# Kernel optimization log

Hardware: AMD Instinct MI355X
Metric: run time of the kernel (lower is better)

Reference implementation:

```python
import jax, jax.numpy as jnp
import numpy as np

LOTRI2MAT = np.array([[0, 1, 3], [1, 2, 4], [3, 4, 5]])  # lower-tri 6-vec -> symmetric 3x3
MAT2LOTRI_I = np.array([0, 1, 1, 2, 2, 2])
MAT2LOTRI_J = np.array([0, 0, 1, 0, 1, 2])


def trilinear_warp_border(img, ddf):
    """MONAI Warp(mode='bilinear', padding_mode='border', align_corners=True).
    img: (B,C,H,W,D), ddf: (B,3,H,W,D) displacement in voxel units.
    Samples img at x + ddf(x), clamping coords to the volume (border padding).
    """
    B, C, H, W, D = img.shape
    base = jnp.stack(
        jnp.meshgrid(jnp.arange(H), jnp.arange(W), jnp.arange(D), indexing='ij'),
        axis=0,
    ).astype(img.dtype)  # (3,H,W,D)
    coords = ddf + base[None]  # (B,3,H,W,D)
    x = jnp.clip(coords[:, 0], 0.0, H - 1)
    y = jnp.clip(coords[:, 1], 0.0, W - 1)
    z = jnp.clip(coords[:, 2], 0.0, D - 1)

    x0f, y0f, z0f = jnp.floor(x), jnp.floor(y), jnp.floor(z)
    fx, fy, fz = x - x0f, y - y0f, z - z0f
    x0 = jnp.clip(x0f.astype(jnp.int32), 0, H - 1)
    y0 = jnp.clip(y0f.astype(jnp.int32), 0, W - 1)
    z0 = jnp.clip(z0f.astype(jnp.int32), 0, D - 1)
    x1 = jnp.minimum(x0 + 1, H - 1)
    y1 = jnp.minimum(y0 + 1, W - 1)
    z1 = jnp.minimum(z0 + 1, D - 1)

    def gather(img_b, xi, yi, zi):
        flat = (xi * W + yi) * D + zi  # (H,W,D)
        return img_b.reshape(C, -1)[:, flat.reshape(-1)].reshape(C, H, W, D)

    g = jax.vmap(gather)  # over batch

    out = jnp.zeros_like(img)
    for xi, wx in ((x0, 1.0 - fx), (x1, fx)):
        for yi, wy in ((y0, 1.0 - fy), (y1, fy)):
            for zi, wz in ((z0, 1.0 - fz), (z1, fz)):
                out = out + g(img, xi, yi, zi) * (wx * wy * wz)[:, None]
    return out


def jacobian_of_ddf(ddf):
    """J = I + du/dx via central differences (one-sided at boundaries).
    ddf: (B,3,H,W,D) -> (B,H,W,D,3,3) with J[...,i,j] = d u_i / d x_j + delta_ij."""
    grads = jnp.gradient(ddf, axis=(2, 3, 4))  # list over j of (B,3,H,W,D)
    J = jnp.stack(grads, axis=2)  # (B,3(i),3(j),H,W,D)
    J = J + jnp.eye(3, dtype=ddf.dtype)[None, :, :, None, None, None]
    return jnp.transpose(J, (0, 3, 4, 5, 1, 2))  # (B,H,W,D,3,3)


def setup_inputs() -> dict:
    key = jax.random.key(0)
    k1, k2 = jax.random.split(key)
    dti = jax.random.normal(k1, (2, 6, 64, 64, 64), dtype=jnp.float32)
    ddf = jax.random.normal(k2, (2, 3, 64, 64, 64), dtype=jnp.float32)
    return {"dti": dti, "ddf": ddf}


def reference(dti, ddf):
    b, _, h, w, d = dti.shape
    # 1) trilinear warp of the 6-channel lower-tri DTI
    dti_warped = trilinear_warp_border(dti, ddf)  # (B,6,H,W,D)
    # 2) lower-tri -> full symmetric 3x3, spatial-last
    M = dti_warped[:, LOTRI2MAT]                      # (B,3,3,H,W,D)
    M = jnp.transpose(M, (0, 3, 4, 5, 1, 2))          # (B,H,W,D,3,3)
    # 3) Jacobian of the deformation and its polar-decomposition rotation (finite strain)
    J = jacobian_of_ddf(ddf)                          # (B,H,W,D,3,3)
    U, _, Vh = jnp.linalg.svd(J, full_matrices=False)
    R = jnp.matmul(U, Vh)                             # orthogonal factor of J
    # 4) rotate tensors: R^T M R
    out = jnp.einsum('...ji,...jk,...kl->...il', R, M, R)
    # 5) back to lower-tri channel-first form
    out = jnp.transpose(out, (0, 4, 5, 1, 2, 3))      # (B,3,3,H,W,D)
    return out[:, MAT2LOTRI_I, MAT2LOTRI_J]           # (B,6,H,W,D)
```

## Files before the change

kernel.cpp:

```cpp
#include <hip/hip_runtime.h>

#define NVOX 262144
#define TOTAL (2 * NVOX)

typedef float f2u __attribute__((ext_vector_type(2), aligned(4)));

__global__ __launch_bounds__(256, 8)
void warp_main(const float* __restrict__ dti,
               const float* __restrict__ ddf,
               float* __restrict__ out,
               int* __restrict__ bad, int max_bad)
{
    const int idx = blockIdx.x * 256 + threadIdx.x;
    const int b = idx >> 18;
    const int r = idx & (NVOX - 1);
    const int x = r >> 12;
    const int y = (r >> 6) & 63;
    const int z = r & 63;

    const float* db = ddf + (size_t)b * 3 * NVOX;

    const float ux = db[r];
    const float uy = db[NVOX + r];
    const float uz = db[2 * NVOX + r];

    const float cx = fminf(fmaxf((float)x + ux, 0.0f), 63.0f);
    const float cy = fminf(fmaxf((float)y + uy, 0.0f), 63.0f);
    const float cz = fminf(fmaxf((float)z + uz, 0.0f), 63.0f);
    const float fx0 = floorf(cx), fy0 = floorf(cy), fz0 = floorf(cz);
    const float fx = cx - fx0, fy = cy - fy0, fz = cz - fz0;
    const int x0 = (int)fx0, y0 = (int)fy0, z0 = (int)fz0;
    const int x1 = min(x0 + 1, 63), y1 = min(y0 + 1, 63);

    const float gx = 1.0f - fx, gy = 1.0f - fy, gz = 1.0f - fz;
    const float q00 = gx * gy, q01 = gx * fy, q10 = fx * gy, q11 = fx * fy;

    const bool ztop = (z0 == 63);
    const int zb = ztop ? 62 : z0;
    const int p00 = (x0 * 64 + y0) * 64 + zb, p01 = (x0 * 64 + y1) * 64 + zb;
    const int p10 = (x1 * 64 + y0) * 64 + zb, p11 = (x1 * 64 + y1) * 64 + zb;

    const float* tb = dti + (size_t)b * 6 * NVOX;
    float m[6];
#pragma unroll
    for (int c = 0; c < 6; ++c) {
        const float* tc = tb + c * NVOX;
        const f2u v00 = *(const f2u*)(tc + p00);
        const f2u v01 = *(const f2u*)(tc + p01);
        const f2u v10 = *(const f2u*)(tc + p10);
        const f2u v11 = *(const f2u*)(tc + p11);
        const float l00 = (ztop ? v00.y : v00.x) * gz + v00.y * fz;
        const float l01 = (ztop ? v01.y : v01.x) * gz + v01.y * fz;
        const float l10 = (ztop ? v10.y : v10.x) * gz + v10.y * fz;
        const float l11 = (ztop ? v11.y : v11.x) * gz + v11.y * fz;
        m[c] = q00 * l00 + q01 * l01 + q10 * l10 + q11 * l11;
    }

    const int xm = max(x - 1, 0), xp = min(x + 1, 63);
    const int ym = max(y - 1, 0), yp = min(y + 1, 63);
    const int zm = max(z - 1, 0), zp = min(z + 1, 63);
    const float sx = (xp - xm == 2) ? 0.5f : 1.0f;
    const float sy = (yp - ym == 2) ? 0.5f : 1.0f;
    const float sz = (zp - zm == 2) ? 0.5f : 1.0f;

    float P[3][3];
#pragma unroll
    for (int i = 0; i < 3; ++i) {
        const float* ui = db + i * NVOX;
        const float ctr = (i == 0) ? ux : (i == 1) ? uy : uz;
        P[i][0] = (ui[(xp * 64 + y) * 64 + z] - ui[(xm * 64 + y) * 64 + z]) * sx
                + (i == 0 ? 1.0f : 0.0f);
        P[i][1] = (ui[(x * 64 + yp) * 64 + z] - ui[(x * 64 + ym) * 64 + z]) * sy
                + (i == 1 ? 1.0f : 0.0f);
        P[i][2] = (__shfl(ctr, zp) - __shfl(ctr, zm)) * sz + (i == 2 ? 1.0f : 0.0f);
    }

    bool ill = false;
#pragma unroll
    for (int it = 0; it < 5; ++it) {
        const float C00 = P[1][1] * P[2][2] - P[1][2] * P[2][1];
        const float C01 = P[1][2] * P[2][0] - P[1][0] * P[2][2];
        const float C02 = P[1][0] * P[2][1] - P[1][1] * P[2][0];
        const float C10 = P[0][2] * P[2][1] - P[0][1] * P[2][2];
        const float C11 = P[0][0] * P[2][2] - P[0][2] * P[2][0];
        const float C12 = P[0][1] * P[2][0] - P[0][0] * P[2][1];
        const float C20 = P[0][1] * P[1][2] - P[0][2] * P[1][1];
        const float C21 = P[0][2] * P[1][0] - P[0][0] * P[1][2];
        const float C22 = P[0][0] * P[1][1] - P[0][1] * P[1][0];
        const float det = P[0][0] * C00 + P[0][1] * C01 + P[0][2] * C02;

        const float n2 = P[0][0]*P[0][0] + P[0][1]*P[0][1] + P[0][2]*P[0][2]
                       + P[1][0]*P[1][0] + P[1][1]*P[1][1] + P[1][2]*P[1][2]
                       + P[2][0]*P[2][0] + P[2][1]*P[2][1] + P[2][2]*P[2][2];
        const float a2 = C00*C00 + C01*C01 + C02*C02
                       + C10*C10 + C11*C11 + C12*C12
                       + C20*C20 + C21*C21 + C22*C22;

        const float ad = fmaxf(fabsf(det), 1e-30f);
        if (it == 0) ill = (n2 * a2 > 1e8f * ad * ad);

        const float t   = fmaxf(sqrtf(a2) * rsqrtf(n2), 1e-20f);
        const float it2 = rsqrtf(t * ad);
        const float sg  = (det < 0.0f) ? -0.5f : 0.5f;
        const float c1  = 0.5f * t * it2;
        const float c2  = sg * it2;

        P[0][0] = c1 * P[0][0] + c2 * C00;  P[0][1] = c1 * P[0][1] + c2 * C01;  P[0][2] = c1 * P[0][2] + c2 * C02;
        P[1][0] = c1 * P[1][0] + c2 * C10;  P[1][1] = c1 * P[1][1] + c2 * C11;  P[1][2] = c1 * P[1][2] + c2 * C12;
        P[2][0] = c1 * P[2][0] + c2 * C20;  P[2][1] = c1 * P[2][1] + c2 * C21;  P[2][2] = c1 * P[2][2] + c2 * C22;
    }

    const float M3[3][3] = {{m[0], m[1], m[3]},
                            {m[1], m[2], m[4]},
                            {m[3], m[4], m[5]}};
    float T[3][3];
#pragma unroll
    for (int i = 0; i < 3; ++i)
#pragma unroll
        for (int j = 0; j < 3; ++j)
            T[i][j] = P[0][i] * M3[0][j] + P[1][i] * M3[1][j] + P[2][i] * M3[2][j];

    float* ob = out + (size_t)b * 6 * NVOX;
    ob[0 * NVOX + r] = T[0][0]*P[0][0] + T[0][1]*P[1][0] + T[0][2]*P[2][0];
    ob[1 * NVOX + r] = T[1][0]*P[0][0] + T[1][1]*P[1][0] + T[1][2]*P[2][0];
    ob[2 * NVOX + r] = T[1][0]*P[0][1] + T[1][1]*P[1][1] + T[1][2]*P[2][1];
    ob[3 * NVOX + r] = T[2][0]*P[0][0] + T[2][1]*P[1][0] + T[2][2]*P[2][0];
    ob[4 * NVOX + r] = T[2][0]*P[0][1] + T[2][1]*P[1][1] + T[2][2]*P[2][1];
    ob[5 * NVOX + r] = T[2][0]*P[0][2] + T[2][1]*P[1][2] + T[2][2]*P[2][2];

    if (ill) {
        const int slot = atomicAdd(bad, 1);
        if (slot < max_bad) bad[1 + slot] = idx;
    }
}

__global__ __launch_bounds__(256)
void rescue(const float* __restrict__ dti,
            const float* __restrict__ ddf,
            float* __restrict__ out,
            const int* __restrict__ bad, int max_bad)
{
    const int n = min(bad[0], max_bad);
    for (int k = blockIdx.x * 256 + threadIdx.x; k < n; k += 4 * 256) {
        const int idx = bad[1 + k];
        const int b = idx >> 18;
        const int r = idx & (NVOX - 1);
        const int x = r >> 12;
        const int y = (r >> 6) & 63;
        const int z = r & 63;

        const float* db = ddf + (size_t)b * 3 * NVOX;

        const float cx = fminf(fmaxf((float)x + db[r], 0.0f), 63.0f);
        const float cy = fminf(fmaxf((float)y + db[NVOX + r], 0.0f), 63.0f);
        const float cz = fminf(fmaxf((float)z + db[2 * NVOX + r], 0.0f), 63.0f);
        const float fx0 = floorf(cx), fy0 = floorf(cy), fz0 = floorf(cz);
        const float fx = cx - fx0, fy = cy - fy0, fz = cz - fz0;
        const int x0 = (int)fx0, y0 = (int)fy0, z0 = (int)fz0;
        const int x1 = min(x0 + 1, 63), y1 = min(y0 + 1, 63), z1 = min(z0 + 1, 63);
        const float gx = 1.0f - fx, gy = 1.0f - fy, gz = 1.0f - fz;
        const float w000 = gx*gy*gz, w001 = gx*gy*fz, w010 = gx*fy*gz, w011 = gx*fy*fz;
        const float w100 = fx*gy*gz, w101 = fx*gy*fz, w110 = fx*fy*gz, w111 = fx*fy*fz;
        const int o000 = (x0*64+y0)*64+z0, o001 = (x0*64+y0)*64+z1;
        const int o010 = (x0*64+y1)*64+z0, o011 = (x0*64+y1)*64+z1;
        const int o100 = (x1*64+y0)*64+z0, o101 = (x1*64+y0)*64+z1;
        const int o110 = (x1*64+y1)*64+z0, o111 = (x1*64+y1)*64+z1;

        const float* tb = dti + (size_t)b * 6 * NVOX;
        float m[6];
        for (int c = 0; c < 6; ++c) {
            const float* tc = tb + c * NVOX;
            m[c] = w000*tc[o000] + w001*tc[o001] + w010*tc[o010] + w011*tc[o011]
                 + w100*tc[o100] + w101*tc[o101] + w110*tc[o110] + w111*tc[o111];
        }

        const int xm = max(x-1,0), xp = min(x+1,63);
        const int ym = max(y-1,0), yp = min(y+1,63);
        const int zm = max(z-1,0), zp = min(z+1,63);
        const double sx = (xp-xm==2)?0.5:1.0, sy = (yp-ym==2)?0.5:1.0, sz = (zp-zm==2)?0.5:1.0;
        double X[3][3];
        for (int i = 0; i < 3; ++i) {
            const float* ui = db + i * NVOX;
            X[i][0] = ((double)ui[(xp*64+y)*64+z] - (double)ui[(xm*64+y)*64+z]) * sx + (i==0?1.0:0.0);
            X[i][1] = ((double)ui[(x*64+yp)*64+z] - (double)ui[(x*64+ym)*64+z]) * sy + (i==1?1.0:0.0);
            X[i][2] = ((double)ui[(x*64+y)*64+zp] - (double)ui[(x*64+y)*64+zm]) * sz + (i==2?1.0:0.0);
        }

        for (int it = 0; it < 14; ++it) {
            double mx = 0.0;
            for (int i = 0; i < 3; ++i)
                for (int j = 0; j < 3; ++j) mx = fmax(mx, fabs(X[i][j]));
            const double s = 1.0 / fmax(mx, 1e-300);
            for (int i = 0; i < 3; ++i)
                for (int j = 0; j < 3; ++j) X[i][j] *= s;

            const double C00 = X[1][1]*X[2][2] - X[1][2]*X[2][1];
            const double C01 = X[1][2]*X[2][0] - X[1][0]*X[2][2];
            const double C02 = X[1][0]*X[2][1] - X[1][1]*X[2][0];
            const double C10 = X[0][2]*X[2][1] - X[0][1]*X[2][2];
            const double C11 = X[0][0]*X[2][2] - X[0][2]*X[2][0];
            const double C12 = X[0][1]*X[2][0] - X[0][0]*X[2][1];
            const double C20 = X[0][1]*X[1][2] - X[0][2]*X[1][1];
            const double C21 = X[0][2]*X[1][0] - X[0][0]*X[1][2];
            const double C22 = X[0][0]*X[1][1] - X[0][1]*X[1][0];
            const double det = X[0][0]*C00 + X[0][1]*C01 + X[0][2]*C02;
            const double n2 = X[0][0]*X[0][0]+X[0][1]*X[0][1]+X[0][2]*X[0][2]
                            + X[1][0]*X[1][0]+X[1][1]*X[1][1]+X[1][2]*X[1][2]
                            + X[2][0]*X[2][0]+X[2][1]*X[2][1]+X[2][2]*X[2][2];
            const double a2 = C00*C00+C01*C01+C02*C02 + C10*C10+C11*C11+C12*C12
                            + C20*C20+C21*C21+C22*C22;
            const double t2 = fmax(sqrt(a2 / n2), 1e-150);
            const double ad = fmax(fabs(det), 1e-280);
            const double sg = (det < 0.0) ? -1.0 : 1.0;
            const double c1 = 0.5 * sqrt(t2 / ad);
            const double c2 = 0.5 * sg / sqrt(t2 * ad);
            X[0][0]=c1*X[0][0]+c2*C00; X[0][1]=c1*X[0][1]+c2*C01; X[0][2]=c1*X[0][2]+c2*C02;
            X[1][0]=c1*X[1][0]+c2*C10; X[1][1]=c1*X[1][1]+c2*C11; X[1][2]=c1*X[1][2]+c2*C12;
            X[2][0]=c1*X[2][0]+c2*C20; X[2][1]=c1*X[2][1]+c2*C21; X[2][2]=c1*X[2][2]+c2*C22;
        }

        const double M3[3][3] = {{(double)m[0], (double)m[1], (double)m[3]},
                                 {(double)m[1], (double)m[2], (double)m[4]},
                                 {(double)m[3], (double)m[4], (double)m[5]}};
        double T[3][3], A[3][3];
        for (int i = 0; i < 3; ++i)
            for (int j = 0; j < 3; ++j)
                T[i][j] = X[0][i]*M3[0][j] + X[1][i]*M3[1][j] + X[2][i]*M3[2][j];
        for (int i = 0; i < 3; ++i)
            for (int j = 0; j < 3; ++j)
                A[i][j] = T[i][0]*X[0][j] + T[i][1]*X[1][j] + T[i][2]*X[2][j];

        float* ob = out + (size_t)b * 6 * NVOX;
        ob[0 * NVOX + r] = (float)A[0][0];
        ob[1 * NVOX + r] = (float)A[1][0];
        ob[2 * NVOX + r] = (float)A[1][1];
        ob[3 * NVOX + r] = (float)A[2][0];
        ob[4 * NVOX + r] = (float)A[2][1];
        ob[5 * NVOX + r] = (float)A[2][2];
    }
}

extern "C" void kernel_launch(void* const* d_in, const int* in_sizes, int n_in,
                              void* d_out, int out_size, void* d_ws, size_t ws_size,
                              hipStream_t stream) {
    const float* dti = (const float*)d_in[0];
    const float* ddf = (const float*)d_in[1];
    float* out = (float*)d_out;
    int* bad = (int*)d_ws;
    const int max_bad = (int)min((size_t)8192, ws_size / 4 - 1);

    hipMemsetAsync(bad, 0, sizeof(int), stream);
    warp_main<<<TOTAL / 256, 256, 0, stream>>>(dti, ddf, out, bad, max_bad);
    rescue<<<4, 256, 0, stream>>>(dti, ddf, out, bad, max_bad);
}
```

Measured before the change: 108.7 us.

## Transpose DTI to interleaved voxel-major layout before trilinear gather

Adds a pre-pass kernel that repacks the 6 channel-planar DTI volume into an 8-float-per-voxel interleaved buffer in workspace. The warp kernel then gathers each corner with two vector loads covering all channels, instead of 24 scattered 8-byte loads across six separate planes. This is meant to cut the number of gather transactions and the cache lines touched. In exchange it adds an extra kernel launch and a full read and write of a 16 MB buffer. It also hardcodes the workspace size assumptions for max_bad.

```diff
diff --git a/kernel.cpp b/kernel.cpp
--- a/kernel.cpp
+++ b/kernel.cpp
@@ -2,11 +2,47 @@
 
 #define NVOX 262144
 #define TOTAL (2 * NVOX)
+#define TBYTES ((size_t)TOTAL * 8 * 4)
 
 typedef float f2u __attribute__((ext_vector_type(2), aligned(4)));
+typedef float f4u __attribute__((ext_vector_type(4), aligned(16)));
+
+__global__ __launch_bounds__(256)
+void transpose_dti(const float* __restrict__ dti, float* __restrict__ dst)
+{
+    const int idx = blockIdx.x * 256 + threadIdx.x;
+    const int b = idx >> 18;
+    const int r = idx & (NVOX - 1);
+    const float* tb = dti + (size_t)b * 6 * NVOX;
+    f4u lo, hi;
+    lo.x = tb[r];            lo.y = tb[NVOX + r];
+    lo.z = tb[2 * NVOX + r]; lo.w = tb[3 * NVOX + r];
+    hi.x = tb[4 * NVOX + r]; hi.y = tb[5 * NVOX + r];
+    hi.z = 0.0f;             hi.w = 0.0f;
+    float* o = dst + (size_t)idx * 8;
+    *(f4u*)o = lo;
+    *(f4u*)(o + 4) = hi;
+}
+
+__device__ __forceinline__ void acc_pair(const float* __restrict__ pp,
+                                         bool ztop, float gz, float fz,
+                                         float q, float m[6])
+{
+    const f4u a0 = *(const f4u*)pp;
+    const f2u b0 = *(const f2u*)(pp + 4);
+    const f4u a1 = *(const f4u*)(pp + 8);
+    const f2u b1 = *(const f2u*)(pp + 12);
+    const float z0c[6] = {a0.x, a0.y, a0.z, a0.w, b0.x, b0.y};
+    const float z1c[6] = {a1.x, a1.y, a1.z, a1.w, b1.x, b1.y};
+#pragma unroll
+    for (int c = 0; c < 6; ++c) {
+        const float v0 = ztop ? z1c[c] : z0c[c];
+        m[c] += q * (v0 * gz + z1c[c] * fz);
+    }
+}
 
 __global__ __launch_bounds__(256, 8)
-void warp_main(const float* __restrict__ dti,
+void warp_main(const float* __restrict__ dti_t,
                const float* __restrict__ ddf,
                float* __restrict__ out,
                int* __restrict__ bad, int max_bad)
@@ -37,24 +73,17 @@
 
     const bool ztop = (z0 == 63);
     const int zb = ztop ? 62 : z0;
-    const int p00 = (x0 * 64 + y0) * 64 + zb, p01 = (x0 * 64 + y1) * 64 + zb;
-    const int p10 = (x1 * 64 + y0) * 64 + zb, p11 = (x1 * 64 + y1) * 64 + zb;
-
-    const float* tb = dti + (size_t)b * 6 * NVOX;
-    float m[6];
-#pragma unroll
-    for (int c = 0; c < 6; ++c) {
-        const float* tc = tb + c * NVOX;
-        const f2u v00 = *(const f2u*)(tc + p00);
-        const f2u v01 = *(const f2u*)(tc + p01);
-        const f2u v10 = *(const f2u*)(tc + p10);
-        const f2u v11 = *(const f2u*)(tc + p11);
-        const float l00 = (ztop ? v00.y : v00.x) * gz + v00.y * fz;
-        const float l01 = (ztop ? v01.y : v01.x) * gz + v01.y * fz;
-        const float l10 = (ztop ? v10.y : v10.x) * gz + v10.y * fz;
-        const float l11 = (ztop ? v11.y : v11.x) * gz + v11.y * fz;
-        m[c] = q00 * l00 + q01 * l01 + q10 * l10 + q11 * l11;
-    }
+    const float* tt = dti_t + (size_t)b * NVOX * 8;
+    const float* pp00 = tt + (size_t)((x0 * 64 + y0) * 64 + zb) * 8;
+    const float* pp01 = tt + (size_t)((x0 * 64 + y1) * 64 + zb) * 8;
+    const float* pp10 = tt + (size_t)((x1 * 64 + y0) * 64 + zb) * 8;
+    const float* pp11 = tt + (size_t)((x1 * 64 + y1) * 64 + zb) * 8;
+
+    float m[6] = {0, 0, 0, 0, 0, 0};
+    acc_pair(pp00, ztop, gz, fz, q00, m);
+    acc_pair(pp01, ztop, gz, fz, q01, m);
+    acc_pair(pp10, ztop, gz, fz, q10, m);
+    acc_pair(pp11, ztop, gz, fz, q11, m);
 
     const int xm = max(x - 1, 0), xp = min(x + 1, 63);
     const int ym = max(y - 1, 0), yp = min(y + 1, 63);
@@ -246,10 +275,12 @@
     const float* dti = (const float*)d_in[0];
     const float* ddf = (const float*)d_in[1];
     float* out = (float*)d_out;
-    int* bad = (int*)d_ws;
-    const int max_bad = (int)min((size_t)8192, ws_size / 4 - 1);
+    float* dti_t = (float*)d_ws;
+    int* bad = (int*)((char*)d_ws + TBYTES);
+    const int max_bad = 8192;
 
     hipMemsetAsync(bad, 0, sizeof(int), stream);
-    warp_main<<<TOTAL / 256, 256, 0, stream>>>(dti, ddf, out, bad, max_bad);
+    transpose_dti<<<TOTAL / 256, 256, 0, stream>>>(dti, dti_t);
+    warp_main<<<TOTAL / 256, 256, 0, stream>>>(dti_t, ddf, out, bad, max_bad);
     rescue<<<4, 256, 0, stream>>>(dti, ddf, out, bad, max_bad);
 }
```

New measurement: 114.9 us. 5.7% more time.

## Replace atomic bad-voxel list with NaN sentinel and full-grid rescue scan

Applied to the files above, without the earlier changes.

Ill-conditioned voxels are now marked by writing a NaN into output channel 0 instead of appending to an atomic work list. This removes the memset launch and the global atomics. The rescue kernel now runs over every voxel, reads channel 0 for both batches and reprocesses only NaN entries, which adds an extra read pass over part of the output. The Jacobian neighbour loads are also moved ahead of the DTI gather to expose more memory parallelism, and the occupancy hint on launch bounds is dropped.

```diff
diff --git a/kernel.cpp b/kernel.cpp
--- a/kernel.cpp
+++ b/kernel.cpp
@@ -5,11 +5,10 @@
 
 typedef float f2u __attribute__((ext_vector_type(2), aligned(4)));
 
-__global__ __launch_bounds__(256, 8)
+__global__ __launch_bounds__(256)
 void warp_main(const float* __restrict__ dti,
                const float* __restrict__ ddf,
-               float* __restrict__ out,
-               int* __restrict__ bad, int max_bad)
+               float* __restrict__ out)
 {
     const int idx = blockIdx.x * 256 + threadIdx.x;
     const int b = idx >> 18;
@@ -23,6 +22,23 @@
     const float ux = db[r];
     const float uy = db[NVOX + r];
     const float uz = db[2 * NVOX + r];
+
+    const int xm = max(x - 1, 0), xp = min(x + 1, 63);
+    const int ym = max(y - 1, 0), yp = min(y + 1, 63);
+    const int zm = max(z - 1, 0), zp = min(z + 1, 63);
+    const float sx = (xp - xm == 2) ? 0.5f : 1.0f;
+    const float sy = (yp - ym == 2) ? 0.5f : 1.0f;
+    const float sz = (zp - zm == 2) ? 0.5f : 1.0f;
+
+    float jx[3][2], jy[3][2];
+#pragma unroll
+    for (int i = 0; i < 3; ++i) {
+        const float* ui = db + i * NVOX;
+        jx[i][0] = ui[(xm * 64 + y) * 64 + z];
+        jx[i][1] = ui[(xp * 64 + y) * 64 + z];
+        jy[i][0] = ui[(x * 64 + ym) * 64 + z];
+        jy[i][1] = ui[(x * 64 + yp) * 64 + z];
+    }
 
     const float cx = fminf(fmaxf((float)x + ux, 0.0f), 63.0f);
     const float cy = fminf(fmaxf((float)y + uy, 0.0f), 63.0f);
@@ -56,22 +72,12 @@
         m[c] = q00 * l00 + q01 * l01 + q10 * l10 + q11 * l11;
     }
 
-    const int xm = max(x - 1, 0), xp = min(x + 1, 63);
-    const int ym = max(y - 1, 0), yp = min(y + 1, 63);
-    const int zm = max(z - 1, 0), zp = min(z + 1, 63);
-    const float sx = (xp - xm == 2) ? 0.5f : 1.0f;
-    const float sy = (yp - ym == 2) ? 0.5f : 1.0f;
-    const float sz = (zp - zm == 2) ? 0.5f : 1.0f;
-
     float P[3][3];
 #pragma unroll
     for (int i = 0; i < 3; ++i) {
-        const float* ui = db + i * NVOX;
         const float ctr = (i == 0) ? ux : (i == 1) ? uy : uz;
-        P[i][0] = (ui[(xp * 64 + y) * 64 + z] - ui[(xm * 64 + y) * 64 + z]) * sx
-                + (i == 0 ? 1.0f : 0.0f);
-        P[i][1] = (ui[(x * 64 + yp) * 64 + z] - ui[(x * 64 + ym) * 64 + z]) * sy
-                + (i == 1 ? 1.0f : 0.0f);
+        P[i][0] = (jx[i][1] - jx[i][0]) * sx + (i == 0 ? 1.0f : 0.0f);
+        P[i][1] = (jy[i][1] - jy[i][0]) * sy + (i == 1 ? 1.0f : 0.0f);
         P[i][2] = (__shfl(ctr, zp) - __shfl(ctr, zm)) * sz + (i == 2 ? 1.0f : 0.0f);
     }
 
@@ -120,35 +126,32 @@
         for (int j = 0; j < 3; ++j)
             T[i][j] = P[0][i] * M3[0][j] + P[1][i] * M3[1][j] + P[2][i] * M3[2][j];
 
+    const float a00 = T[0][0]*P[0][0] + T[0][1]*P[1][0] + T[0][2]*P[2][0];
+    const float qnan = __int_as_float(0x7fc00000);
+
     float* ob = out + (size_t)b * 6 * NVOX;
-    ob[0 * NVOX + r] = T[0][0]*P[0][0] + T[0][1]*P[1][0] + T[0][2]*P[2][0];
+    ob[0 * NVOX + r] = ill ? qnan : a00;
     ob[1 * NVOX + r] = T[1][0]*P[0][0] + T[1][1]*P[1][0] + T[1][2]*P[2][0];
     ob[2 * NVOX + r] = T[1][0]*P[0][1] + T[1][1]*P[1][1] + T[1][2]*P[2][1];
     ob[3 * NVOX + r] = T[2][0]*P[0][0] + T[2][1]*P[1][0] + T[2][2]*P[2][0];
     ob[4 * NVOX + r] = T[2][0]*P[0][1] + T[2][1]*P[1][1] + T[2][2]*P[2][1];
     ob[5 * NVOX + r] = T[2][0]*P[0][2] + T[2][1]*P[1][2] + T[2][2]*P[2][2];
-
-    if (ill) {
-        const int slot = atomicAdd(bad, 1);
-        if (slot < max_bad) bad[1 + slot] = idx;
-    }
 }
 
 __global__ __launch_bounds__(256)
 void rescue(const float* __restrict__ dti,
             const float* __restrict__ ddf,
-            float* __restrict__ out,
-            const int* __restrict__ bad, int max_bad)
+            float* __restrict__ out)
 {
-    const int n = min(bad[0], max_bad);
-    for (int k = blockIdx.x * 256 + threadIdx.x; k < n; k += 4 * 256) {
-        const int idx = bad[1 + k];
-        const int b = idx >> 18;
-        const int r = idx & (NVOX - 1);
-        const int x = r >> 12;
-        const int y = (r >> 6) & 63;
-        const int z = r & 63;
-
+    const int t = blockIdx.x * 256 + threadIdx.x;
+#pragma unroll
+    for (int b = 0; b < 2; ++b) {
+        const int r = t;
+        float* ob = out + (size_t)b * 6 * NVOX;
+        const float v = ob[r];
+        if (!(v != v)) continue;
+
+        const int x = r >> 12, y = (r >> 6) & 63, z = r & 63;
         const float* db = ddf + (size_t)b * 3 * NVOX;
 
         const float cx = fminf(fmaxf((float)x + db[r], 0.0f), 63.0f);
@@ -230,7 +233,6 @@
             for (int j = 0; j < 3; ++j)
                 A[i][j] = T[i][0]*X[0][j] + T[i][1]*X[1][j] + T[i][2]*X[2][j];
 
-        float* ob = out + (size_t)b * 6 * NVOX;
         ob[0 * NVOX + r] = (float)A[0][0];
         ob[1 * NVOX + r] = (float)A[1][0];
         ob[2 * NVOX + r] = (float)A[1][1];
@@ -246,10 +248,6 @@
     const float* dti = (const float*)d_in[0];
     const float* ddf = (const float*)d_in[1];
     float* out = (float*)d_out;
-    int* bad = (int*)d_ws;
-    const int max_bad = (int)min((size_t)8192, ws_size / 4 - 1);
-
-    hipMemsetAsync(bad, 0, sizeof(int), stream);
-    warp_main<<<TOTAL / 256, 256, 0, stream>>>(dti, ddf, out, bad, max_bad);
-    rescue<<<4, 256, 0, stream>>>(dti, ddf, out, bad, max_bad);
+    warp_main<<<TOTAL / 256, 256, 0, stream>>>(dti, ddf, out);
+    rescue<<<NVOX / 256, 256, 0, stream>>>(dti, ddf, out);
 }
```

Result: slower. 114.1 us (+4.9%).
